# Optimization experiments

Hardware: AMD Instinct MI355X
Metric: run time of the kernel (lower is better)

The kernel has to match this reference:

```python
import jax, jax.numpy as jnp
import numpy as np

T = 0.2          # temperature
W = 0.1          # loss weight
BIG = 2 ** 30    # sentinel label for masked-out samples


def setup_inputs() -> dict:
    key = jax.random.key(0)
    k1, k2, k3, k4 = jax.random.split(key, 4)
    bs, C, Gn, S = 32, 128, 256, 16
    grouped_features = jax.random.normal(k1, (bs, C, Gn, S), dtype=jnp.float32)
    # instance labels in [-1, 8): -1 = background
    proposal_instance_mask = jax.random.randint(k2, (bs, Gn, S), -1, 8, dtype=jnp.int32)
    # seed indices with duplicates possible (range 40 over 16 samples)
    grouped_indices = jax.random.randint(k3, (bs, Gn, S), 0, 40, dtype=jnp.int32)
    context_compen = jax.random.normal(k4, (1, C), dtype=jnp.float32)
    return {
        "proposal_instance_mask": proposal_instance_mask,
        "grouped_features": grouped_features,
        "grouped_indices": grouped_indices,
        "context_compen": context_compen,
    }


def _group_loss(feat, idx, lab, ctx):
    # feat: [S, C], idx: [S], lab: [S], ctx: [C]
    # NOTE: sum_{a,b} f_a . g_b / (n_f * n_g) == mean(f) . mean(g), so the
    # original tiny-mm contrastive loss reduces to pairwise dots of per-instance means.
    S, C = feat.shape
    pos = jnp.arange(S)
    # unique count of seed indices -> truncate to first u samples (as in torch code)
    si = jnp.sort(idx)
    u = 1 + jnp.sum(si[1:] != si[:-1])
    valid = pos < u
    lab_m = jnp.where(valid, lab, BIG)
    # per-group unique labels (sorted), jit-friendly
    sl = jnp.sort(lab_m)
    new = jnp.concatenate([jnp.ones((1,), bool), sl[1:] != sl[:-1]])
    cid = jnp.cumsum(new) - 1                      # compact id of each sorted label
    uniq = jnp.full((S,), BIG, sl.dtype).at[cid].set(sl)
    n_labels = jnp.sum(new & (sl != BIG))          # number of distinct valid labels
    has_bg = uniq[0] == -1                         # -1 sorts first if present
    # per-instance mean features via segment scatter-add
    comp = jnp.searchsorted(uniq, lab_m)           # sample -> compact instance slot
    sums = jnp.zeros((S, C), feat.dtype).at[comp].add(jnp.where(valid[:, None], feat, 0.0))
    cnts = jnp.zeros((S,), feat.dtype).at[comp].add(valid.astype(feat.dtype))
    means = sums / jnp.maximum(cnts, 1.0)[:, None]
    hb = has_bg.astype(jnp.int32)
    fg_count = n_labels - hb
    inst_num = fg_count + 1                        # bg slot always present
    # row 0 = bg mean (or context_compen if no bg), rows 1.. = fg means
    gidx = jnp.clip(pos + hb - 1, 0, S - 1)
    M = means[gidx]
    M = M.at[0].set(jnp.where(has_bg, M[0], ctx))
    inst_valid = pos < inst_num
    sim = (M @ M.T) / T                            # [S, S] tiny matmul of means
    sim_m = jnp.where(inst_valid[None, :], sim, -jnp.inf)
    lse = jax.scipy.special.logsumexp(sim_m, axis=1)
    li = lse - jnp.diagonal(sim)                   # -log(pos/(pos+neg)) per fg row
    fg_mask = inst_valid & (pos >= 1)
    gl = jnp.sum(jnp.where(fg_mask, li, 0.0)) / jnp.maximum(inst_num - 1, 1).astype(feat.dtype)
    return gl, fg_count >= 1


def reference(proposal_instance_mask, grouped_features, grouped_indices, context_compen):
    bs, C, Gn, S = grouped_features.shape
    feats = grouped_features.transpose(0, 2, 3, 1).reshape(-1, S, C)  # [G, S, C]
    idxs = grouped_indices.reshape(-1, S)
    labs = proposal_instance_mask.reshape(-1, S)
    ctx = context_compen[0]
    gl, gv = jax.vmap(lambda f, i, l: _group_loss(f, i, l, ctx))(feats, idxs, labs)
    gvf = gv.astype(gl.dtype)
    return jnp.sum(gl * gvf) / jnp.sum(gvf) * W
```

## Files before the change

### kernel.cpp

```cpp
#include <hip/hip_runtime.h>

#define GQ    8192
#define BLKG  8
#define NBLK  (GQ / BLKG)
#define MROW  132
#define STG   (64 * MROW)
#define SIMW  72
#define SQRT5 2.23606797749978969f

__global__ __launch_bounds__(64 * BLKG, 8) void group_loss_kernel(
    const int*   __restrict__ labs,
    const float* __restrict__ feats,
    const int*   __restrict__ idxs,
    const float* __restrict__ ctx,
    float2*      __restrict__ ws)
{
    __shared__ float SH[STG + BLKG * SIMW];

    const int l  = threadIdx.x & 63;
    const int w  = threadIdx.x >> 6;
    const int g0 = blockIdx.x * BLKG;
    const int g  = g0 + w;
    const int b  = g0 >> 8;
    const int gn0 = g0 & 255;
    float* SIM = SH + STG + w * SIMW;

    const float* base = feats + (long)b * 524288 + (long)gn0 * 16;
    const int lo = l & 31;

    int myidx = -1, mylab = -2;
    if (l < 16) { myidx = idxs[g * 16 + l]; mylab = labs[g * 16 + l]; }
    const float cx0 = ctx[l], cx1 = ctx[l + 64];

    #pragma unroll
    for (int k = 0; k < 4; ++k) {
        const int ch = w * 8 + k * 2 + (l >> 5);
        const float4 v = *(const float4*)(base + (long)ch * 4096 + lo * 4);
        *(float4*)(SH + ch * MROW + lo * 4) = v;
    }

    unsigned long long mm = ~0ull;
    #pragma unroll
    for (int bit = 0; bit < 6; ++bit) {
        const unsigned long long bb = __ballot((myidx >> bit) & 1);
        mm &= ((myidx >> bit) & 1) ? bb : ~bb;
    }
    const bool dup = (mm & ((1ull << l) - 1) & 0xFFFFull) != 0ull;
    const int u = __popcll(__ballot((l < 16) && !dup));

    const bool valid = l < u;
    const int bid = valid ? (mylab + 1) : 255;

    int cnt9[9];
    #pragma unroll
    for (int r = 0; r < 9; ++r) cnt9[r] = __popcll(__ballot(bid == r));
    const bool has_bg = cnt9[0] > 0;
    int fg_count = 0, pm = 0;
    #pragma unroll
    for (int r = 1; r < 9; ++r)
        if (cnt9[r] > 0) { ++fg_count; pm |= 1 << r; }

    float m0[9] = {0,0,0,0,0,0,0,0,0};
    float m1[9] = {0,0,0,0,0,0,0,0,0};

    __syncthreads();
    {
        const float* R = SH + l * MROW + w * 16;
        #pragma unroll
        for (int q = 0; q < 4; ++q) {
            const float4 x = *(const float4*)(R + 4 * q);
            #pragma unroll
            for (int e = 0; e < 4; ++e) {
                const int s = 4 * q + e;
                if (s < u) {
                    const int bs = __builtin_amdgcn_readlane(bid, s);
                    const float v = (e == 0) ? x.x : (e == 1) ? x.y
                                  : (e == 2) ? x.z : x.w;
                    switch (bs) {
                        case 0: m0[0] += v; break;  case 1: m0[1] += v; break;
                        case 2: m0[2] += v; break;  case 3: m0[3] += v; break;
                        case 4: m0[4] += v; break;  case 5: m0[5] += v; break;
                        case 6: m0[6] += v; break;  case 7: m0[7] += v; break;
                        case 8: m0[8] += v; break;
                    }
                }
            }
        }
    }
    __syncthreads();

    #pragma unroll
    for (int k = 0; k < 4; ++k) {
        const int ch = w * 8 + k * 2 + (l >> 5);
        const float4 v = *(const float4*)(base + (long)(64 + ch) * 4096 + lo * 4);
        *(float4*)(SH + ch * MROW + lo * 4) = v;
    }
    __syncthreads();

    {
        const float* R = SH + l * MROW + w * 16;
        #pragma unroll
        for (int q = 0; q < 4; ++q) {
            const float4 x = *(const float4*)(R + 4 * q);
            #pragma unroll
            for (int e = 0; e < 4; ++e) {
                const int s = 4 * q + e;
                if (s < u) {
                    const int bs = __builtin_amdgcn_readlane(bid, s);
                    const float v = (e == 0) ? x.x : (e == 1) ? x.y
                                  : (e == 2) ? x.z : x.w;
                    switch (bs) {
                        case 0: m1[0] += v; break;  case 1: m1[1] += v; break;
                        case 2: m1[2] += v; break;  case 3: m1[3] += v; break;
                        case 4: m1[4] += v; break;  case 5: m1[5] += v; break;
                        case 6: m1[6] += v; break;  case 7: m1[7] += v; break;
                        case 8: m1[8] += v; break;
                    }
                }
            }
        }
    }

    #pragma unroll
    for (int r = 0; r < 9; ++r) {
        const float sc = SQRT5 / (float)(cnt9[r] > 0 ? cnt9[r] : 1);
        m0[r] *= sc; m1[r] *= sc;
    }
    if (!has_bg) { m0[0] = cx0 * SQRT5; m1[0] = cx1 * SQRT5; }

    #pragma unroll
    for (int r = 1; r <= 8; ++r) {
        float p[8];
        #pragma unroll
        for (int j = 0; j < 8; ++j)
            p[j] = m0[r] * m0[j] + m1[r] * m1[j];
        #pragma unroll
        for (int i = 0; i < 4; ++i) {
            const float send = (l & 32) ? p[i] : p[i + 4];
            const float recv = __shfl_xor(send, 32);
            p[i] = ((l & 32) ? p[i + 4] : p[i]) + recv;
        }
        #pragma unroll
        for (int i = 0; i < 2; ++i) {
            const float send = (l & 16) ? p[i] : p[i + 2];
            const float recv = __shfl_xor(send, 16);
            p[i] = ((l & 16) ? p[i + 2] : p[i]) + recv;
        }
        {
            const float send = (l & 8) ? p[0] : p[1];
            const float recv = __shfl_xor(send, 8);
            p[0] = ((l & 8) ? p[1] : p[0]) + recv;
        }
        p[0] += __shfl_xor(p[0], 4);
        p[0] += __shfl_xor(p[0], 2);
        p[0] += __shfl_xor(p[0], 1);
        if ((l & 7) == 0) SIM[(r - 1) * 8 + (l >> 3)] = p[0];
    }
    float s88 = m0[8] * m0[8] + m1[8] * m1[8];
    s88 += __shfl_xor(s88, 1);  s88 += __shfl_xor(s88, 2);
    s88 += __shfl_xor(s88, 4);  s88 += __shfl_xor(s88, 8);
    s88 += __shfl_xor(s88, 16); s88 += __shfl_xor(s88, 32);

    const int cm = pm | 1;
    const float NINF = __int_as_float(0xFF800000);
    float li = 0.0f;
    if (l >= 1 && l <= 8) {
        const float* Rw = SIM + (l - 1) * 8;
        const float4 ra = *(const float4*)(Rw);
        const float4 rb = *(const float4*)(Rw + 4);
        const float s8 = SIM[56 + l];
        float srow[9] = { ra.x, ra.y, ra.z, ra.w, rb.x, rb.y, rb.z, rb.w,
                          (l == 8) ? s88 : s8 };
        float vmax = NINF, diag = 0.0f, v[9];
        #pragma unroll
        for (int j = 0; j < 9; ++j) {
            v[j] = ((cm >> j) & 1) ? srow[j] : NINF;
            vmax = fmaxf(vmax, v[j]);
            if (j >= 1) diag = (l == j) ? srow[j] : diag;
        }
        float se = 0.0f;
        #pragma unroll
        for (int j = 0; j < 9; ++j) se += __expf(v[j] - vmax);
        li = vmax + __logf(se) - diag;
        li = ((pm >> l) & 1) ? li : 0.0f;
    }

    float ssum = li;
    ssum += __shfl_down(ssum, 8);
    ssum += __shfl_down(ssum, 4);
    ssum += __shfl_down(ssum, 2);
    ssum += __shfl_down(ssum, 1);
    if (l == 0) {
        float2 r;
        r.x = ssum / (float)(fg_count > 0 ? fg_count : 1);
        r.y = (fg_count > 0) ? 1.0f : 0.0f;
        ws[g] = r;
    }
}

__global__ __launch_bounds__(1024) void reduce_kernel(
    const float2* __restrict__ ws, float* __restrict__ out)
{
    __shared__ float sa[1024], sb[1024];
    const int t = threadIdx.x;
    float a = 0.0f, b2 = 0.0f;
    for (int g = t; g < GQ; g += 1024) {
        float2 v = ws[g];
        a += v.x; b2 += v.y;
    }
    sa[t] = a; sb[t] = b2;
    __syncthreads();
    for (int off = 512; off > 0; off >>= 1) {
        if (t < off) { sa[t] += sa[t + off]; sb[t] += sb[t + off]; }
        __syncthreads();
    }
    if (t == 0) out[0] = 0.1f * (sa[0] / sb[0]);
}

extern "C" void kernel_launch(void* const* d_in, const int* in_sizes, int n_in,
                              void* d_out, int out_size, void* d_ws, size_t ws_size,
                              hipStream_t stream) {
    const int*   labs  = (const int*)d_in[0];
    const float* feats = (const float*)d_in[1];
    const int*   idxs  = (const int*)d_in[2];
    const float* ctx   = (const float*)d_in[3];
    float* out = (float*)d_out;
    float2* ws = (float2*)d_ws;

    group_loss_kernel<<<NBLK, 64 * BLKG, 0, stream>>>(labs, feats, idxs, ctx, ws);
    reduce_kernel<<<1, 1024, 0, stream>>>(ws, out);
}
```

Before: 110.0 us.

## Prefetch second channel half into registers during first reduction; use DPP reductions

The global loads for the second 64 channels are now issued into registers before the first shared-memory reduction pass, so their latency overlaps with the segment-sum compute instead of being serialized after a barrier. The first-half loads are also hoisted before the ballot/label logic. Some butterfly shuffles are replaced with DPP row operations, and the full-wave sum uses a DPP scan plus a readlane. This adds register pressure from the 4 float4 staging values and relies on DPP control encodings being correct.

```diff
diff --git a/kernel.cpp b/kernel.cpp
--- a/kernel.cpp
+++ b/kernel.cpp
@@ -7,6 +7,21 @@
 #define STG   (64 * MROW)
 #define SIMW  72
 #define SQRT5 2.23606797749978969f
+
+template<int CTRL>
+__device__ __forceinline__ float dpp_add(float v) {
+    int t = __builtin_amdgcn_update_dpp(0, __float_as_int(v), CTRL, 0xF, 0xF, true);
+    return v + __int_as_float(t);
+}
+__device__ __forceinline__ float wave_sum64(float v) {
+    v = dpp_add<0x111>(v);
+    v = dpp_add<0x112>(v);
+    v = dpp_add<0x114>(v);
+    v = dpp_add<0x118>(v);
+    v = dpp_add<0x142>(v);
+    v = dpp_add<0x143>(v);
+    return v;
+}
 
 __global__ __launch_bounds__(64 * BLKG, 8) void group_loss_kernel(
     const int*   __restrict__ labs,
@@ -27,17 +42,16 @@
 
     const float* base = feats + (long)b * 524288 + (long)gn0 * 16;
     const int lo = l & 31;
+    const int ch = w * 8 + (l >> 5);
 
     int myidx = -1, mylab = -2;
     if (l < 16) { myidx = idxs[g * 16 + l]; mylab = labs[g * 16 + l]; }
     const float cx0 = ctx[l], cx1 = ctx[l + 64];
 
-    #pragma unroll
-    for (int k = 0; k < 4; ++k) {
-        const int ch = w * 8 + k * 2 + (l >> 5);
-        const float4 v = *(const float4*)(base + (long)ch * 4096 + lo * 4);
-        *(float4*)(SH + ch * MROW + lo * 4) = v;
-    }
+    float4 st[4];
+    #pragma unroll
+    for (int k = 0; k < 4; ++k)
+        st[k] = *(const float4*)(base + (long)(ch + 2 * k) * 4096 + lo * 4);
 
     unsigned long long mm = ~0ull;
     #pragma unroll
@@ -60,10 +74,19 @@
     for (int r = 1; r < 9; ++r)
         if (cnt9[r] > 0) { ++fg_count; pm |= 1 << r; }
 
+    #pragma unroll
+    for (int k = 0; k < 4; ++k)
+        *(float4*)(SH + (ch + 2 * k) * MROW + lo * 4) = st[k];
+    __syncthreads();
+
+    #pragma unroll
+    for (int k = 0; k < 4; ++k)
+        st[k] = *(const float4*)(base + (long)(64 + ch + 2 * k) * 4096 + lo * 4);
+    __builtin_amdgcn_sched_barrier(0);
+
     float m0[9] = {0,0,0,0,0,0,0,0,0};
     float m1[9] = {0,0,0,0,0,0,0,0,0};
 
-    __syncthreads();
     {
         const float* R = SH + l * MROW + w * 16;
         #pragma unroll
@@ -90,11 +113,8 @@
     __syncthreads();
 
     #pragma unroll
-    for (int k = 0; k < 4; ++k) {
-        const int ch = w * 8 + k * 2 + (l >> 5);
-        const float4 v = *(const float4*)(base + (long)(64 + ch) * 4096 + lo * 4);
-        *(float4*)(SH + ch * MROW + lo * 4) = v;
-    }
+    for (int k = 0; k < 4; ++k)
+        *(float4*)(SH + (ch + 2 * k) * MROW + lo * 4) = st[k];
     __syncthreads();
 
     {
@@ -152,14 +172,12 @@
             p[0] = ((l & 8) ? p[1] : p[0]) + recv;
         }
         p[0] += __shfl_xor(p[0], 4);
-        p[0] += __shfl_xor(p[0], 2);
-        p[0] += __shfl_xor(p[0], 1);
+        p[0] = dpp_add<0x4E>(p[0]);
+        p[0] = dpp_add<0xB1>(p[0]);
         if ((l & 7) == 0) SIM[(r - 1) * 8 + (l >> 3)] = p[0];
     }
-    float s88 = m0[8] * m0[8] + m1[8] * m1[8];
-    s88 += __shfl_xor(s88, 1);  s88 += __shfl_xor(s88, 2);
-    s88 += __shfl_xor(s88, 4);  s88 += __shfl_xor(s88, 8);
-    s88 += __shfl_xor(s88, 16); s88 += __shfl_xor(s88, 32);
+    float s88 = wave_sum64(m0[8] * m0[8] + m1[8] * m1[8]);
+    s88 = __int_as_float(__builtin_amdgcn_readlane(__float_as_int(s88), 63));
 
     const int cm = pm | 1;
     const float NINF = __int_as_float(0xFF800000);
```

Result: slower. 125.3 us (+13.8%).

## Use one wave per group, load features directly and accumulate Gram terms in registers

Applied to the files above, without the earlier changes.

Each group now gets its own 64-thread block. Lanes load float4s directly from global memory, four lanes per channel covering the 16 samples, instead of staging through a shared-memory transpose. Per-lane label codes built from ballots select which instance sum each sample goes into. DPP adds reduce across the four lanes, and the 44 unique pairwise dot products are accumulated in registers across 8 channel chunks. The block index is remapped to interleave batches, and the reduce loop is unrolled. The cost is high register pressure (44 plus 9 accumulators) and 4-lane-wide coalescing on global loads, in exchange for removing LDS staging and block-wide barriers.

```diff
diff --git a/kernel.cpp b/kernel.cpp
--- a/kernel.cpp
+++ b/kernel.cpp
@@ -1,43 +1,34 @@
 #include <hip/hip_runtime.h>
 
 #define GQ    8192
-#define BLKG  8
-#define NBLK  (GQ / BLKG)
-#define MROW  132
-#define STG   (64 * MROW)
-#define SIMW  72
-#define SQRT5 2.23606797749978969f
-
-__global__ __launch_bounds__(64 * BLKG, 8) void group_loss_kernel(
+#define C14   1.11803398874989485f
+
+template<int CTRL>
+__device__ __forceinline__ float dpp_add(float v) {
+    int t = __builtin_amdgcn_update_dpp(0, __float_as_int(v), CTRL, 0xF, 0xF, true);
+    return v + __int_as_float(t);
+}
+
+__global__ __launch_bounds__(64, 4) void group_loss_kernel(
     const int*   __restrict__ labs,
     const float* __restrict__ feats,
     const int*   __restrict__ idxs,
     const float* __restrict__ ctx,
     float2*      __restrict__ ws)
 {
-    __shared__ float SH[STG + BLKG * SIMW];
-
-    const int l  = threadIdx.x & 63;
-    const int w  = threadIdx.x >> 6;
-    const int g0 = blockIdx.x * BLKG;
-    const int g  = g0 + w;
-    const int b  = g0 >> 8;
-    const int gn0 = g0 & 255;
-    float* SIM = SH + STG + w * SIMW;
-
-    const float* base = feats + (long)b * 524288 + (long)gn0 * 16;
-    const int lo = l & 31;
+    __shared__ float SIM[72];
+
+    const int l   = threadIdx.x;
+    const int blk = blockIdx.x;
+    const int g   = ((blk & 7) << 10) | (blk >> 3);
+    const int b   = g >> 8;
+    const int gn  = g & 255;
+    const long fbase = (long)b * 524288 + (long)gn * 16;
+    const int ch0   = l >> 2;
+    const int sbase = (l & 3) * 4;
 
     int myidx = -1, mylab = -2;
     if (l < 16) { myidx = idxs[g * 16 + l]; mylab = labs[g * 16 + l]; }
-    const float cx0 = ctx[l], cx1 = ctx[l + 64];
-
-    #pragma unroll
-    for (int k = 0; k < 4; ++k) {
-        const int ch = w * 8 + k * 2 + (l >> 5);
-        const float4 v = *(const float4*)(base + (long)ch * 4096 + lo * 4);
-        *(float4*)(SH + ch * MROW + lo * 4) = v;
-    }
 
     unsigned long long mm = ~0ull;
     #pragma unroll
@@ -49,7 +40,7 @@
     const int u = __popcll(__ballot((l < 16) && !dup));
 
     const bool valid = l < u;
-    const int bid = valid ? (mylab + 1) : 255;
+    const int bid = valid ? (mylab + 1) : 15;
 
     int cnt9[9];
     #pragma unroll
@@ -60,80 +51,71 @@
     for (int r = 1; r < 9; ++r)
         if (cnt9[r] > 0) { ++fg_count; pm |= 1 << r; }
 
-    float m0[9] = {0,0,0,0,0,0,0,0,0};
-    float m1[9] = {0,0,0,0,0,0,0,0,0};
-
-    __syncthreads();
-    {
-        const float* R = SH + l * MROW + w * 16;
-        #pragma unroll
-        for (int q = 0; q < 4; ++q) {
-            const float4 x = *(const float4*)(R + 4 * q);
+    unsigned bm[4];
+    #pragma unroll
+    for (int bit = 0; bit < 4; ++bit)
+        bm[bit] = (unsigned)__ballot((bid >> bit) & 1);
+    int code[4];
+    #pragma unroll
+    for (int k = 0; k < 4; ++k) {
+        const int s = sbase + k;
+        code[k] = ((bm[0] >> s) & 1) | (((bm[1] >> s) & 1) << 1)
+                | (((bm[2] >> s) & 1) << 2) | (((bm[3] >> s) & 1) << 3);
+    }
+
+    float sc[9];
+    #pragma unroll
+    for (int r = 0; r < 9; ++r)
+        sc[r] = C14 / (float)(cnt9[r] > 0 ? cnt9[r] : 1);
+    float ctxv[8];
+    #pragma unroll
+    for (int k = 0; k < 8; ++k) ctxv[k] = ctx[ch0 + 16 * k];
+
+    const int PI_[44] = {1,1, 2,2,2, 3,3,3,3, 4,4,4,4,4, 5,5,5,5,5,5,
+                         6,6,6,6,6,6,6, 7,7,7,7,7,7,7,7, 8,8,8,8,8,8,8,8,8};
+    const int PJ_[44] = {0,1, 0,1,2, 0,1,2,3, 0,1,2,3,4, 0,1,2,3,4,5,
+                         0,1,2,3,4,5,6, 0,1,2,3,4,5,6,7, 0,1,2,3,4,5,6,7,8};
+    float simp[44];
+    #pragma unroll
+    for (int k = 0; k < 44; ++k) simp[k] = 0.0f;
+
+    #pragma unroll
+    for (int k = 0; k < 8; ++k) {
+        const float4 v = *(const float4*)(feats + fbase
+                            + (long)(ch0 + 16 * k) * 4096 + sbase);
+        float acc[9];
+        #pragma unroll
+        for (int r = 0; r < 9; ++r) acc[r] = 0.0f;
+        #pragma unroll
+        for (int e = 0; e < 4; ++e) {
+            const float x = (e == 0) ? v.x : (e == 1) ? v.y : (e == 2) ? v.z : v.w;
+            const int  c = code[e];
             #pragma unroll
-            for (int e = 0; e < 4; ++e) {
-                const int s = 4 * q + e;
-                if (s < u) {
-                    const int bs = __builtin_amdgcn_readlane(bid, s);
-                    const float v = (e == 0) ? x.x : (e == 1) ? x.y
-                                  : (e == 2) ? x.z : x.w;
-                    switch (bs) {
-                        case 0: m0[0] += v; break;  case 1: m0[1] += v; break;
-                        case 2: m0[2] += v; break;  case 3: m0[3] += v; break;
-                        case 4: m0[4] += v; break;  case 5: m0[5] += v; break;
-                        case 6: m0[6] += v; break;  case 7: m0[7] += v; break;
-                        case 8: m0[8] += v; break;
-                    }
-                }
-            }
-        }
-    }
-    __syncthreads();
-
-    #pragma unroll
-    for (int k = 0; k < 4; ++k) {
-        const int ch = w * 8 + k * 2 + (l >> 5);
-        const float4 v = *(const float4*)(base + (long)(64 + ch) * 4096 + lo * 4);
-        *(float4*)(SH + ch * MROW + lo * 4) = v;
-    }
-    __syncthreads();
-
-    {
-        const float* R = SH + l * MROW + w * 16;
-        #pragma unroll
-        for (int q = 0; q < 4; ++q) {
-            const float4 x = *(const float4*)(R + 4 * q);
-            #pragma unroll
-            for (int e = 0; e < 4; ++e) {
-                const int s = 4 * q + e;
-                if (s < u) {
-                    const int bs = __builtin_amdgcn_readlane(bid, s);
-                    const float v = (e == 0) ? x.x : (e == 1) ? x.y
-                                  : (e == 2) ? x.z : x.w;
-                    switch (bs) {
-                        case 0: m1[0] += v; break;  case 1: m1[1] += v; break;
-                        case 2: m1[2] += v; break;  case 3: m1[3] += v; break;
-                        case 4: m1[4] += v; break;  case 5: m1[5] += v; break;
-                        case 6: m1[6] += v; break;  case 7: m1[7] += v; break;
-                        case 8: m1[8] += v; break;
-                    }
-                }
-            }
-        }
-    }
-
-    #pragma unroll
-    for (int r = 0; r < 9; ++r) {
-        const float sc = SQRT5 / (float)(cnt9[r] > 0 ? cnt9[r] : 1);
-        m0[r] *= sc; m1[r] *= sc;
-    }
-    if (!has_bg) { m0[0] = cx0 * SQRT5; m1[0] = cx1 * SQRT5; }
-
+            for (int r = 0; r < 9; ++r)
+                acc[r] += (c == r) ? x : 0.0f;
+        }
+        float m[9];
+        #pragma unroll
+        for (int r = 0; r < 9; ++r) {
+            float t = dpp_add<0xB1>(acc[r]);
+            t = dpp_add<0x4E>(t);
+            m[r] = t * sc[r];
+        }
+        m[0] = has_bg ? m[0] : ctxv[k] * C14;
+        #pragma unroll
+        for (int p = 0; p < 44; ++p)
+            simp[p] += m[PI_[p]] * m[PJ_[p]];
+    }
+
+    const int OFF_[9] = {0, 0, 2, 5, 9, 14, 20, 27, 35};
     #pragma unroll
     for (int r = 1; r <= 8; ++r) {
         float p[8];
         #pragma unroll
-        for (int j = 0; j < 8; ++j)
-            p[j] = m0[r] * m0[j] + m1[r] * m1[j];
+        for (int j = 0; j < 8; ++j) {
+            const int idx = (j <= r) ? (OFF_[r] + j) : (OFF_[j] + r);
+            p[j] = simp[idx];
+        }
         #pragma unroll
         for (int i = 0; i < 4; ++i) {
             const float send = (l & 32) ? p[i] : p[i + 4];
@@ -152,14 +134,16 @@
             p[0] = ((l & 8) ? p[1] : p[0]) + recv;
         }
         p[0] += __shfl_xor(p[0], 4);
-        p[0] += __shfl_xor(p[0], 2);
-        p[0] += __shfl_xor(p[0], 1);
+        p[0] = dpp_add<0x4E>(p[0]);
+        p[0] = dpp_add<0xB1>(p[0]);
         if ((l & 7) == 0) SIM[(r - 1) * 8 + (l >> 3)] = p[0];
     }
-    float s88 = m0[8] * m0[8] + m1[8] * m1[8];
+    float s88 = simp[43];
     s88 += __shfl_xor(s88, 1);  s88 += __shfl_xor(s88, 2);
     s88 += __shfl_xor(s88, 4);  s88 += __shfl_xor(s88, 8);
     s88 += __shfl_xor(s88, 16); s88 += __shfl_xor(s88, 32);
+
+    __syncthreads();
 
     const int cm = pm | 1;
     const float NINF = __int_as_float(0xFF800000);
@@ -171,16 +155,16 @@
         const float s8 = SIM[56 + l];
         float srow[9] = { ra.x, ra.y, ra.z, ra.w, rb.x, rb.y, rb.z, rb.w,
                           (l == 8) ? s88 : s8 };
-        float vmax = NINF, diag = 0.0f, v[9];
+        float vmax = NINF, diag = 0.0f, vv[9];
         #pragma unroll
         for (int j = 0; j < 9; ++j) {
-            v[j] = ((cm >> j) & 1) ? srow[j] : NINF;
-            vmax = fmaxf(vmax, v[j]);
+            vv[j] = ((cm >> j) & 1) ? srow[j] : NINF;
+            vmax = fmaxf(vmax, vv[j]);
             if (j >= 1) diag = (l == j) ? srow[j] : diag;
         }
         float se = 0.0f;
         #pragma unroll
-        for (int j = 0; j < 9; ++j) se += __expf(v[j] - vmax);
+        for (int j = 0; j < 9; ++j) se += __expf(vv[j] - vmax);
         li = vmax + __logf(se) - diag;
         li = ((pm >> l) & 1) ? li : 0.0f;
     }
@@ -204,8 +188,9 @@
     __shared__ float sa[1024], sb[1024];
     const int t = threadIdx.x;
     float a = 0.0f, b2 = 0.0f;
-    for (int g = t; g < GQ; g += 1024) {
-        float2 v = ws[g];
+    #pragma unroll
+    for (int i = 0; i < GQ / 1024; ++i) {
+        const float2 v = ws[t + i * 1024];
         a += v.x; b2 += v.y;
     }
     sa[t] = a; sb[t] = b2;
@@ -227,6 +212,6 @@
     float* out = (float*)d_out;
     float2* ws = (float2*)d_ws;
 
-    group_loss_kernel<<<NBLK, 64 * BLKG, 0, stream>>>(labs, feats, idxs, ctx, ws);
+    group_loss_kernel<<<GQ, 64, 0, stream>>>(labs, feats, idxs, ctx, ws);
     reduce_kernel<<<1, 1024, 0, stream>>>(ws, out);
 }
```

Result: slower. 116.5 us (+5.8%).
